# Kernel optimization log

Measured on AMD Instinct MI355X. Metric: run time of the kernel, lower is better.

Reference implementation:

```python
import jax, jax.numpy as jnp
import numpy as np

T, H, I, E, K = 4096, 2048, 1408, 8, 2  # tokens, hidden, intermediate, experts, top_k


def setup_inputs() -> dict:
    key = jax.random.key(0)
    ks = jax.random.split(key, 6)
    hidden_states = jax.random.normal(ks[0], (T, H), dtype=jnp.float32)
    gate_weight = jax.random.normal(ks[1], (E, H), dtype=jnp.float32) * 0.02  # fp32 gate, per source assert
    w13_weight = jax.random.randint(ks[2], (E, 2 * I, H), -127, 128, dtype=jnp.int8)
    w13_weight_scale = jax.random.uniform(ks[3], (E, 2 * I), dtype=jnp.float32, minval=0.5, maxval=1.5) * 0.005
    w2_weight = jax.random.randint(ks[4], (E, H, I), -127, 128, dtype=jnp.int8)
    w2_weight_scale = jax.random.uniform(ks[5], (E, H), dtype=jnp.float32, minval=0.5, maxval=1.5) * 0.005
    return dict(hidden_states=hidden_states, gate_weight=gate_weight,
                w13_weight=w13_weight, w13_weight_scale=w13_weight_scale,
                w2_weight=w2_weight, w2_weight_scale=w2_weight_scale)


def _dynamic_quant_i8(x):
    # per-token dynamic symmetric int8: scale = max|x|/127 (smooth scales default to ones)
    s = jnp.maximum(jnp.max(jnp.abs(x), axis=-1, keepdims=True) / 127.0, 1e-8)
    q = jnp.clip(jnp.round(x / s), -127.0, 127.0)
    return q, s


def reference(hidden_states, gate_weight, w13_weight, w13_weight_scale, w2_weight, w2_weight_scale):
    # --- gating: fp32 linear + topk softmax (renormalize=True) ---
    logits = hidden_states @ gate_weight.T              # [T, E]
    probs = jax.nn.softmax(logits, axis=-1)
    topv, topi = jax.lax.top_k(probs, K)                # [T, K]
    gates = topv / jnp.sum(topv, axis=-1, keepdims=True)
    # dense routing weights [T, E]: gate value where expert selected, else 0
    route = jnp.zeros((T, E), hidden_states.dtype).at[jnp.arange(T)[:, None], topi].add(gates)

    # --- dynamic per-token int8 quant of routed input (same token value for each of its K copies) ---
    q_in, s_in = _dynamic_quant_i8(hidden_states)       # [T, H], [T, 1]

    # --- grouped w8a8 GEMM (fc1) -> SwiGLU -> requant -> grouped GEMM (fc2) -> weighted combine ---
    def step(acc, xs):
        w13, s13, w2, s2w, r = xs                       # per-expert weights / route column [T]
        h1 = (q_in @ w13.T.astype(jnp.float32)) * s_in * s13[None, :]   # dequant fc1: [T, 2I]
        g, u = h1[:, :I], h1[:, I:]
        act = jax.nn.silu(g) * u                        # SwiGLU
        q_a, s_a = _dynamic_quant_i8(act)
        h2 = (q_a @ w2.T.astype(jnp.float32)) * s_a * s2w[None, :]      # dequant fc2: [T, H]
        return acc + r[:, None] * h2, None

    acc0 = jnp.zeros_like(hidden_states)
    out, _ = jax.lax.scan(step, acc0,
                          (w13_weight, w13_weight_scale, w2_weight, w2_weight_scale, route.T))
    return out
```

## Files before the change

kernel.cpp:

```cpp
#include <hip/hip_runtime.h>

#define T_TOK 4096
#define H_DIM 2048
#define I_DIM 1408
#define E_NUM 8
#define NI2   (2 * I_DIM)

typedef int v4i __attribute__((ext_vector_type(4)));

#define GLD_LDS16(gptr, lptr)                                                        \
  __builtin_amdgcn_global_load_lds(                                                  \
      (const __attribute__((address_space(1))) void*)(gptr),                         \
      (__attribute__((address_space(3))) void*)(lptr), 16, 0, 0)

__global__ __launch_bounds__(256) void pack_all(const int* __restrict__ w13,
                                                const int* __restrict__ w2,
                                                signed char* __restrict__ qw13,
                                                signed char* __restrict__ qw2,
                                                int n16a, int n16tot) {
  int i = blockIdx.x * 256 + threadIdx.x;
  if (i >= n16tot) return;
  const int* src;
  signed char* dst;
  int j;
  if (i < n16a) { src = w13; dst = qw13; j = i; }
  else          { src = w2;  dst = qw2;  j = i - n16a; }
  const int4* s4 = (const int4*)src + (size_t)j * 4;
  int4 v0 = s4[0], v1 = s4[1], v2 = s4[2], v3 = s4[3];
  union { signed char c[16]; int4 v; } pk;
  pk.c[0] = (signed char)v0.x;  pk.c[1] = (signed char)v0.y;
  pk.c[2] = (signed char)v0.z;  pk.c[3] = (signed char)v0.w;
  pk.c[4] = (signed char)v1.x;  pk.c[5] = (signed char)v1.y;
  pk.c[6] = (signed char)v1.z;  pk.c[7] = (signed char)v1.w;
  pk.c[8] = (signed char)v2.x;  pk.c[9] = (signed char)v2.y;
  pk.c[10] = (signed char)v2.z; pk.c[11] = (signed char)v2.w;
  pk.c[12] = (signed char)v3.x; pk.c[13] = (signed char)v3.y;
  pk.c[14] = (signed char)v3.z; pk.c[15] = (signed char)v3.w;
  ((int4*)dst)[j] = pk.v;
}

__global__ __launch_bounds__(256) void gate_route_quant(
    const float* __restrict__ hs, const float* __restrict__ gw,
    signed char* __restrict__ qin, float* __restrict__ s_in,
    int* __restrict__ tope, float* __restrict__ gts) {
  const int t = blockIdx.x;
  const int tid = threadIdx.x;
  const int lane = tid & 63;
  const int wave = tid >> 6;
  const float* row = hs + (size_t)t * H_DIM;

  const float4* r4 = (const float4*)row + tid * 2;
  float4 xa = r4[0], xb = r4[1];
  float x[8] = {xa.x, xa.y, xa.z, xa.w, xb.x, xb.y, xb.z, xb.w};

  double pd[8];
  for (int e = 0; e < 8; e++) pd[e] = 0.0;
  float am = 0.f;
  for (int j = 0; j < 8; j++) {
    float v = x[j];
    am = fmaxf(am, fabsf(v));
    int col = tid * 8 + j;
    for (int e = 0; e < 8; e++)
      pd[e] += (double)v * (double)gw[e * H_DIM + col];
  }
  for (int e = 0; e < 8; e++)
    for (int s = 32; s; s >>= 1) pd[e] += __shfl_down(pd[e], s);
  for (int s = 32; s; s >>= 1) am = fmaxf(am, __shfl_down(am, s));

  __shared__ double sred[4][8];
  __shared__ float sam[4];
  __shared__ float sbc;
  if (lane == 0) {
    for (int e = 0; e < 8; e++) sred[wave][e] = pd[e];
    sam[wave] = am;
  }
  __syncthreads();
  if (tid == 0) {
    float l[8];
    for (int e = 0; e < 8; e++)
      l[e] = (float)(sred[0][e] + sred[1][e] + sred[2][e] + sred[3][e]);
    float amx = fmaxf(fmaxf(sam[0], sam[1]), fmaxf(sam[2], sam[3]));
    float s = fmaxf(amx / 127.0f, 1e-8f);
    s_in[t] = s;
    sbc = s;
    int i1 = 0;
    for (int e = 1; e < 8; e++) if (l[e] > l[i1]) i1 = e;
    int i2 = -1;
    for (int e = 0; e < 8; e++) {
      if (e == i1) continue;
      if (i2 < 0 || l[e] > l[i2]) i2 = e;
    }
    float d = expf(l[i2] - l[i1]);
    tope[2 * t] = i1;     gts[2 * t] = 1.0f / (1.0f + d);
    tope[2 * t + 1] = i2; gts[2 * t + 1] = d / (1.0f + d);
  }
  __syncthreads();
  float s = sbc;
  union { signed char c[8]; unsigned long long u; } pk;
  for (int j = 0; j < 8; j++) {
    float q = rintf(x[j] / s);
    q = fminf(127.f, fmaxf(-127.f, q));
    pk.c[j] = (signed char)q;
  }
  ((unsigned long long*)(qin + (size_t)t * H_DIM))[tid] = pk.u;
}

__global__ __launch_bounds__(256) void build_lists(
    const int* __restrict__ tope, int* __restrict__ tok_list,
    int* __restrict__ epos, int* __restrict__ cnt) {
  const int e = blockIdx.x;
  const int tid = threadIdx.x;
  const int lane = tid & 63;
  const int wave = tid >> 6;
  __shared__ int wsum[4];
  __shared__ int base_s;
  if (tid == 0) base_s = 0;
  __syncthreads();
  for (int t0 = 0; t0 < T_TOK; t0 += 256) {
    int t = t0 + tid;
    int i1 = tope[2 * t], i2 = tope[2 * t + 1];
    int slot = (i1 == e) ? 0 : ((i2 == e) ? 1 : -1);
    unsigned long long m = __ballot(slot >= 0);
    int wpre = __popcll(m & ((1ull << lane) - 1ull));
    if (lane == 0) wsum[wave] = __popcll(m);
    __syncthreads();
    int pre = wpre;
    for (int w = 0; w < wave; w++) pre += wsum[w];
    int total = wsum[0] + wsum[1] + wsum[2] + wsum[3];
    int b = base_s;
    if (slot >= 0) {
      int pos = b + pre;
      tok_list[e * T_TOK + pos] = t;
      epos[2 * t + slot] = (e << 16) | pos;
    }
    __syncthreads();
    if (tid == 0) base_s = b + total;
  }
  __syncthreads();
  if (tid == 0) cnt[e] = base_s;
}

__global__ void calc_off(const int* __restrict__ cnt, int* __restrict__ off) {
  if (threadIdx.x == 0) {
    int s = 0;
    for (int e = 0; e < E_NUM; e++) { off[e] = s; s += cnt[e]; }
  }
}

__global__ __launch_bounds__(256, 3) void gemm1_silu(
    const signed char* __restrict__ qw13, const signed char* __restrict__ qin,
    const float* __restrict__ s_in, const float* __restrict__ s13,
    const int* __restrict__ tok_list, const int* __restrict__ cnt,
    const int* __restrict__ off, float* __restrict__ act,
    unsigned int* __restrict__ amax) {
  const int e = blockIdx.z;
  const int ce = cnt[e];
  const int m0 = blockIdx.y * 64;
  if (m0 >= ce) return;
  const int n0 = blockIdx.x * 128;

  __shared__ __align__(16) signed char As[64 * 64];
  __shared__ __align__(16) signed char Bg[128 * 64];
  __shared__ __align__(16) signed char Bu[128 * 64];

  const int tid = threadIdx.x;
  const int lane = tid & 63;
  const int wave = tid >> 6;
  const int quad = lane >> 4;
  const int ln = lane & 15;

  const int* tl = tok_list + e * T_TOK;
  const int rowA = tid >> 2;
  const int kc = (tid & 3) * 16;

  const int tA = tl[min(m0 + rowA, ce - 1)];
  const signed char* gA = qin + (size_t)tA * H_DIM + kc;
  const signed char* w13e = qw13 + (size_t)e * NI2 * H_DIM;
  const signed char* gBg0 = w13e + (size_t)(n0 + rowA) * H_DIM + kc;
  const signed char* gBg1 = w13e + (size_t)(n0 + rowA + 64) * H_DIM + kc;
  const signed char* gBu0 = gBg0 + (size_t)I_DIM * H_DIM;
  const signed char* gBu1 = gBg1 + (size_t)I_DIM * H_DIM;
  const int ldsA = tid * 16;
  const int lds1 = 4096 + ldsA;

  v4i accg[4][2], accu[4][2];
  v4i zero = {0, 0, 0, 0};
#pragma unroll
  for (int i = 0; i < 4; i++)
#pragma unroll
    for (int j = 0; j < 2; j++) { accg[i][j] = zero; accu[i][j] = zero; }

  for (int k0 = 0; k0 < H_DIM; k0 += 64) {
    __syncthreads();
    GLD_LDS16(gA + k0, As + ldsA);
    GLD_LDS16(gBg0 + k0, Bg + ldsA);
    GLD_LDS16(gBg1 + k0, Bg + lds1);
    GLD_LDS16(gBu0 + k0, Bu + ldsA);
    GLD_LDS16(gBu1 + k0, Bu + lds1);
    __syncthreads();

    v4i af[4], bgf[2], buf_[2];
#pragma unroll
    for (int mt = 0; mt < 4; mt++)
      af[mt] = *(const v4i*)(As + (mt * 16 + ln) * 64 + quad * 16);
#pragma unroll
    for (int nt = 0; nt < 2; nt++) {
      bgf[nt] = *(const v4i*)(Bg + (wave * 32 + nt * 16 + ln) * 64 + quad * 16);
      buf_[nt] = *(const v4i*)(Bu + (wave * 32 + nt * 16 + ln) * 64 + quad * 16);
    }
#pragma unroll
    for (int mt = 0; mt < 4; mt++)
#pragma unroll
      for (int nt = 0; nt < 2; nt++) {
        accg[mt][nt] = __builtin_amdgcn_mfma_i32_16x16x64_i8(af[mt], bgf[nt], accg[mt][nt], 0, 0, 0);
        accu[mt][nt] = __builtin_amdgcn_mfma_i32_16x16x64_i8(af[mt], buf_[nt], accu[mt][nt], 0, 0, 0);
      }
  }

  const float* s13e = s13 + e * NI2;
  float sg[2], su[2];
  int ncol[2];
#pragma unroll
  for (int nt = 0; nt < 2; nt++) {
    int n = n0 + wave * 32 + nt * 16 + ln;
    ncol[nt] = n;
    sg[nt] = s13e[n];
    su[nt] = s13e[I_DIM + n];
  }
  const int offe = off[e];
#pragma unroll
  for (int mt = 0; mt < 4; mt++) {
#pragma unroll
    for (int r = 0; r < 4; r++) {
      int mrel = m0 + mt * 16 + quad * 4 + r;
      bool valid = mrel < ce;
      int tok = tl[valid ? mrel : 0];
      float si = s_in[tok];
      int crow = offe + mrel;
      float* arow = act + (size_t)crow * I_DIM;
      float am = 0.f;
#pragma unroll
      for (int nt = 0; nt < 2; nt++) {
        float g = (float)accg[mt][nt][r] * si * sg[nt];
        float u = (float)accu[mt][nt][r] * si * su[nt];
        float a = g / (1.0f + expf(-g)) * u;
        if (valid) arow[ncol[nt]] = a;
        am = fmaxf(am, fabsf(a));
      }
      for (int s = 1; s < 16; s <<= 1) am = fmaxf(am, __shfl_xor(am, s, 16));
      if (valid && ln == 0) atomicMax(amax + crow, __float_as_uint(am));
    }
  }
}

__global__ __launch_bounds__(256) void quant_act(const float* __restrict__ act,
                                                 const unsigned int* __restrict__ amax,
                                                 signed char* __restrict__ qa,
                                                 float* __restrict__ s_a) {
  const int r = blockIdx.x;
  float am = __uint_as_float(amax[r]);
  float s = fmaxf(am / 127.0f, 1e-8f);
  if (threadIdx.x == 0) s_a[r] = s;
  const float* arow = act + (size_t)r * I_DIM;
  signed char* qrow = qa + (size_t)r * I_DIM;
  for (int j = threadIdx.x; j < I_DIM; j += 256) {
    float q = rintf(arow[j] / s);
    q = fminf(127.f, fmaxf(-127.f, q));
    qrow[j] = (signed char)q;
  }
}

__global__ __launch_bounds__(256, 4) void gemm2_h2(
    const signed char* __restrict__ qw2, const signed char* __restrict__ qa,
    const float* __restrict__ s_a, const float* __restrict__ s2w,
    const int* __restrict__ cnt, const int* __restrict__ off,
    float* __restrict__ h2s) {
  const int e = blockIdx.z;
  const int ce = cnt[e];
  const int m0 = blockIdx.y * 64;
  if (m0 >= ce) return;
  const int n0 = blockIdx.x * 128;
  const int offe = off[e];

  __shared__ __align__(16) signed char As[64 * 64];
  __shared__ __align__(16) signed char Bs[128 * 64];

  const int tid = threadIdx.x;
  const int lane = tid & 63;
  const int wave = tid >> 6;
  const int quad = lane >> 4;
  const int ln = lane & 15;

  const int rowA = tid >> 2;
  const int kc = (tid & 3) * 16;

  const signed char* gA = qa + (size_t)(offe + min(m0 + rowA, ce - 1)) * I_DIM + kc;
  const signed char* w2e = qw2 + (size_t)e * H_DIM * I_DIM;
  const signed char* gB0 = w2e + (size_t)(n0 + rowA) * I_DIM + kc;
  const signed char* gB1 = w2e + (size_t)(n0 + rowA + 64) * I_DIM + kc;
  const int ldsA = tid * 16;
  const int lds1 = 4096 + ldsA;

  v4i acc[4][2];
  v4i zero = {0, 0, 0, 0};
#pragma unroll
  for (int i = 0; i < 4; i++)
#pragma unroll
    for (int j = 0; j < 2; j++) acc[i][j] = zero;

  for (int k0 = 0; k0 < I_DIM; k0 += 64) {
    __syncthreads();
    GLD_LDS16(gA + k0, As + ldsA);
    GLD_LDS16(gB0 + k0, Bs + ldsA);
    GLD_LDS16(gB1 + k0, Bs + lds1);
    __syncthreads();

    v4i af[4], bf[2];
#pragma unroll
    for (int mt = 0; mt < 4; mt++)
      af[mt] = *(const v4i*)(As + (mt * 16 + ln) * 64 + quad * 16);
#pragma unroll
    for (int nt = 0; nt < 2; nt++)
      bf[nt] = *(const v4i*)(Bs + (wave * 32 + nt * 16 + ln) * 64 + quad * 16);
#pragma unroll
    for (int mt = 0; mt < 4; mt++)
#pragma unroll
      for (int nt = 0; nt < 2; nt++)
        acc[mt][nt] = __builtin_amdgcn_mfma_i32_16x16x64_i8(af[mt], bf[nt], acc[mt][nt], 0, 0, 0);
  }

  const float* s2e = s2w + e * H_DIM;
  float sw[2];
  int ncol[2];
#pragma unroll
  for (int nt = 0; nt < 2; nt++) {
    int n = n0 + wave * 32 + nt * 16 + ln;
    ncol[nt] = n;
    sw[nt] = s2e[n];
  }
#pragma unroll
  for (int mt = 0; mt < 4; mt++) {
#pragma unroll
    for (int r = 0; r < 4; r++) {
      int mrel = m0 + mt * 16 + quad * 4 + r;
      if (mrel >= ce) continue;
      float sa = s_a[offe + mrel];
      float* orow = h2s + (size_t)(offe + mrel) * H_DIM;
#pragma unroll
      for (int nt = 0; nt < 2; nt++)
        orow[ncol[nt]] = (float)acc[mt][nt][r] * sa * sw[nt];
    }
  }
}

__global__ __launch_bounds__(256) void gather_out(
    const float* __restrict__ h2s, const int* __restrict__ epos,
    const float* __restrict__ gts, const int* __restrict__ off,
    float* __restrict__ out) {
  const int t = blockIdx.x;
  int a = epos[2 * t], b = epos[2 * t + 1];
  float g1 = gts[2 * t], g2 = gts[2 * t + 1];
  int r1 = off[a >> 16] + (a & 0xffff);
  int r2 = off[b >> 16] + (b & 0xffff);
  const float4* R1 = (const float4*)(h2s + (size_t)r1 * H_DIM);
  const float4* R2 = (const float4*)(h2s + (size_t)r2 * H_DIM);
  float4* O = (float4*)(out + (size_t)t * H_DIM);
  for (int c = threadIdx.x; c < H_DIM / 4; c += 256) {
    float4 x = R1[c], y = R2[c];
    float4 z;
    z.x = g1 * x.x + g2 * y.x;
    z.y = g1 * x.y + g2 * y.y;
    z.z = g1 * x.z + g2 * y.z;
    z.w = g1 * x.w + g2 * y.w;
    O[c] = z;
  }
}

extern "C" void kernel_launch(void* const* d_in, const int* in_sizes, int n_in,
                              void* d_out, int out_size, void* d_ws, size_t ws_size,
                              hipStream_t stream) {
  const float* hs = (const float*)d_in[0];
  const float* gw = (const float*)d_in[1];
  const int* w13 = (const int*)d_in[2];
  const float* s13 = (const float*)d_in[3];
  const int* w2 = (const int*)d_in[4];
  const float* s2w = (const float*)d_in[5];
  float* out = (float*)d_out;

  char* ws = (char*)d_ws;
  size_t o = 0;
  auto take = [&](size_t b) {
    char* p = ws + o;
    o += (b + 255) & ~(size_t)255;
    return p;
  };
  signed char* qw13 = (signed char*)take((size_t)E_NUM * NI2 * H_DIM);
  signed char* qin = (signed char*)take((size_t)T_TOK * H_DIM);
  float* act = (float*)take((size_t)T_TOK * 2 * I_DIM * 4);
  float* h2s = (float*)qw13;
  signed char* qw2 = (signed char*)take((size_t)E_NUM * H_DIM * I_DIM);
  signed char* qa = (signed char*)take((size_t)T_TOK * 2 * I_DIM);
  float* sin_ = (float*)take((size_t)T_TOK * 4);
  float* sa = (float*)take((size_t)T_TOK * 2 * 4);
  unsigned int* amax = (unsigned int*)take((size_t)T_TOK * 2 * 4);
  int* tokl = (int*)take((size_t)E_NUM * T_TOK * 4);
  int* tope = (int*)take((size_t)T_TOK * 2 * 4);
  int* epos = (int*)take((size_t)T_TOK * 2 * 4);
  float* gts = (float*)take((size_t)T_TOK * 2 * 4);
  int* cnt = (int*)take(E_NUM * 4);
  int* off = (int*)take(E_NUM * 4);

  hipMemsetAsync(amax, 0, (size_t)T_TOK * 2 * 4, stream);

  {
    int n16a = E_NUM * NI2 * H_DIM / 16;
    int n16b = E_NUM * H_DIM * I_DIM / 16;
    int n16tot = n16a + n16b;
    pack_all<<<(n16tot + 255) / 256, 256, 0, stream>>>(w13, w2, qw13, qw2, n16a, n16tot);
  }
  gate_route_quant<<<T_TOK, 256, 0, stream>>>(hs, gw, qin, sin_, tope, gts);
  build_lists<<<E_NUM, 256, 0, stream>>>(tope, tokl, epos, cnt);
  calc_off<<<1, 64, 0, stream>>>(cnt, off);
  {
    dim3 g(I_DIM / 128, T_TOK / 64, E_NUM);
    gemm1_silu<<<g, 256, 0, stream>>>(qw13, qin, sin_, s13, tokl, cnt, off, act, amax);
  }
  quant_act<<<T_TOK * 2, 256, 0, stream>>>(act, amax, qa, sa);
  {
    dim3 g(H_DIM / 128, T_TOK / 64, E_NUM);
    gemm2_h2<<<g, 256, 0, stream>>>(qw2, qa, sa, s2w, cnt, off, h2s);
  }
  gather_out<<<T_TOK, 256, 0, stream>>>(h2s, epos, gts, off, out);
}
```

Baseline: 582.4 us.

## Parallelize list building and interleave experts in flattened GEMM grids

build_lists now runs one block per 256 tokens, using shared-memory atomics for per-expert slot positions and global atomics on a zeroed count array, replacing the sequential per-expert scan across all tokens. Both grouped GEMMs switch to a 1D grid with the expert index in the low bits, so blocks from different experts interleave and early-exiting empty tiles are spread out. gemm1 also halves its N tile to 64 columns and raises the occupancy hint to 4 blocks per CU, which gives more blocks for load balance but less B reuse per A load. Token order within each expert list becomes nondeterministic, which is harmless for correctness since positions are recorded in epos.

```diff
diff --git a/kernel.cpp b/kernel.cpp
--- a/kernel.cpp
+++ b/kernel.cpp
@@ -108,36 +108,24 @@
 __global__ __launch_bounds__(256) void build_lists(
     const int* __restrict__ tope, int* __restrict__ tok_list,
     int* __restrict__ epos, int* __restrict__ cnt) {
-  const int e = blockIdx.x;
+  __shared__ int lc[E_NUM];
+  __shared__ int lbase[E_NUM];
   const int tid = threadIdx.x;
-  const int lane = tid & 63;
-  const int wave = tid >> 6;
-  __shared__ int wsum[4];
-  __shared__ int base_s;
-  if (tid == 0) base_s = 0;
+  if (tid < E_NUM) lc[tid] = 0;
   __syncthreads();
-  for (int t0 = 0; t0 < T_TOK; t0 += 256) {
-    int t = t0 + tid;
-    int i1 = tope[2 * t], i2 = tope[2 * t + 1];
-    int slot = (i1 == e) ? 0 : ((i2 == e) ? 1 : -1);
-    unsigned long long m = __ballot(slot >= 0);
-    int wpre = __popcll(m & ((1ull << lane) - 1ull));
-    if (lane == 0) wsum[wave] = __popcll(m);
-    __syncthreads();
-    int pre = wpre;
-    for (int w = 0; w < wave; w++) pre += wsum[w];
-    int total = wsum[0] + wsum[1] + wsum[2] + wsum[3];
-    int b = base_s;
-    if (slot >= 0) {
-      int pos = b + pre;
-      tok_list[e * T_TOK + pos] = t;
-      epos[2 * t + slot] = (e << 16) | pos;
-    }
-    __syncthreads();
-    if (tid == 0) base_s = b + total;
-  }
+  const int t = blockIdx.x * 256 + tid;
+  int e0 = tope[2 * t], e1 = tope[2 * t + 1];
+  int p0 = atomicAdd(&lc[e0], 1);
+  int p1 = atomicAdd(&lc[e1], 1);
   __syncthreads();
-  if (tid == 0) cnt[e] = base_s;
+  if (tid < E_NUM) lbase[tid] = atomicAdd(&cnt[tid], lc[tid]);
+  __syncthreads();
+  int pos0 = lbase[e0] + p0;
+  int pos1 = lbase[e1] + p1;
+  tok_list[e0 * T_TOK + pos0] = t;
+  tok_list[e1 * T_TOK + pos1] = t;
+  epos[2 * t] = (e0 << 16) | pos0;
+  epos[2 * t + 1] = (e1 << 16) | pos1;
 }
 
 __global__ void calc_off(const int* __restrict__ cnt, int* __restrict__ off) {
@@ -147,21 +135,24 @@
   }
 }
 
-__global__ __launch_bounds__(256, 3) void gemm1_silu(
+__global__ __launch_bounds__(256, 4) void gemm1_silu(
     const signed char* __restrict__ qw13, const signed char* __restrict__ qin,
     const float* __restrict__ s_in, const float* __restrict__ s13,
     const int* __restrict__ tok_list, const int* __restrict__ cnt,
     const int* __restrict__ off, float* __restrict__ act,
     unsigned int* __restrict__ amax) {
-  const int e = blockIdx.z;
+  const int bid = blockIdx.x;
+  const int e = bid & 7;
+  const int xt = bid >> 9;
+  const int yt = (bid >> 3) & 63;
   const int ce = cnt[e];
-  const int m0 = blockIdx.y * 64;
+  const int m0 = yt * 64;
   if (m0 >= ce) return;
-  const int n0 = blockIdx.x * 128;
+  const int n0 = xt * 64;
 
   __shared__ __align__(16) signed char As[64 * 64];
-  __shared__ __align__(16) signed char Bg[128 * 64];
-  __shared__ __align__(16) signed char Bu[128 * 64];
+  __shared__ __align__(16) signed char Bg[64 * 64];
+  __shared__ __align__(16) signed char Bu[64 * 64];
 
   const int tid = threadIdx.x;
   const int lane = tid & 63;
@@ -176,57 +167,39 @@
   const int tA = tl[min(m0 + rowA, ce - 1)];
   const signed char* gA = qin + (size_t)tA * H_DIM + kc;
   const signed char* w13e = qw13 + (size_t)e * NI2 * H_DIM;
-  const signed char* gBg0 = w13e + (size_t)(n0 + rowA) * H_DIM + kc;
-  const signed char* gBg1 = w13e + (size_t)(n0 + rowA + 64) * H_DIM + kc;
-  const signed char* gBu0 = gBg0 + (size_t)I_DIM * H_DIM;
-  const signed char* gBu1 = gBg1 + (size_t)I_DIM * H_DIM;
+  const signed char* gBg = w13e + (size_t)(n0 + rowA) * H_DIM + kc;
+  const signed char* gBu = gBg + (size_t)I_DIM * H_DIM;
   const int ldsA = tid * 16;
-  const int lds1 = 4096 + ldsA;
-
-  v4i accg[4][2], accu[4][2];
+
+  v4i accg[4], accu[4];
   v4i zero = {0, 0, 0, 0};
 #pragma unroll
-  for (int i = 0; i < 4; i++)
-#pragma unroll
-    for (int j = 0; j < 2; j++) { accg[i][j] = zero; accu[i][j] = zero; }
+  for (int i = 0; i < 4; i++) { accg[i] = zero; accu[i] = zero; }
 
   for (int k0 = 0; k0 < H_DIM; k0 += 64) {
     __syncthreads();
     GLD_LDS16(gA + k0, As + ldsA);
-    GLD_LDS16(gBg0 + k0, Bg + ldsA);
-    GLD_LDS16(gBg1 + k0, Bg + lds1);
-    GLD_LDS16(gBu0 + k0, Bu + ldsA);
-    GLD_LDS16(gBu1 + k0, Bu + lds1);
+    GLD_LDS16(gBg + k0, Bg + ldsA);
+    GLD_LDS16(gBu + k0, Bu + ldsA);
     __syncthreads();
 
-    v4i af[4], bgf[2], buf_[2];
+    v4i af[4], bg, bu;
 #pragma unroll
     for (int mt = 0; mt < 4; mt++)
       af[mt] = *(const v4i*)(As + (mt * 16 + ln) * 64 + quad * 16);
-#pragma unroll
-    for (int nt = 0; nt < 2; nt++) {
-      bgf[nt] = *(const v4i*)(Bg + (wave * 32 + nt * 16 + ln) * 64 + quad * 16);
-      buf_[nt] = *(const v4i*)(Bu + (wave * 32 + nt * 16 + ln) * 64 + quad * 16);
+    bg = *(const v4i*)(Bg + (wave * 16 + ln) * 64 + quad * 16);
+    bu = *(const v4i*)(Bu + (wave * 16 + ln) * 64 + quad * 16);
+#pragma unroll
+    for (int mt = 0; mt < 4; mt++) {
+      accg[mt] = __builtin_amdgcn_mfma_i32_16x16x64_i8(af[mt], bg, accg[mt], 0, 0, 0);
+      accu[mt] = __builtin_amdgcn_mfma_i32_16x16x64_i8(af[mt], bu, accu[mt], 0, 0, 0);
     }
-#pragma unroll
-    for (int mt = 0; mt < 4; mt++)
-#pragma unroll
-      for (int nt = 0; nt < 2; nt++) {
-        accg[mt][nt] = __builtin_amdgcn_mfma_i32_16x16x64_i8(af[mt], bgf[nt], accg[mt][nt], 0, 0, 0);
-        accu[mt][nt] = __builtin_amdgcn_mfma_i32_16x16x64_i8(af[mt], buf_[nt], accu[mt][nt], 0, 0, 0);
-      }
   }
 
   const float* s13e = s13 + e * NI2;
-  float sg[2], su[2];
-  int ncol[2];
-#pragma unroll
-  for (int nt = 0; nt < 2; nt++) {
-    int n = n0 + wave * 32 + nt * 16 + ln;
-    ncol[nt] = n;
-    sg[nt] = s13e[n];
-    su[nt] = s13e[I_DIM + n];
-  }
+  const int n = n0 + wave * 16 + ln;
+  const float sgv = s13e[n];
+  const float suv = s13e[I_DIM + n];
   const int offe = off[e];
 #pragma unroll
   for (int mt = 0; mt < 4; mt++) {
@@ -237,16 +210,11 @@
       int tok = tl[valid ? mrel : 0];
       float si = s_in[tok];
       int crow = offe + mrel;
-      float* arow = act + (size_t)crow * I_DIM;
-      float am = 0.f;
-#pragma unroll
-      for (int nt = 0; nt < 2; nt++) {
-        float g = (float)accg[mt][nt][r] * si * sg[nt];
-        float u = (float)accu[mt][nt][r] * si * su[nt];
-        float a = g / (1.0f + expf(-g)) * u;
-        if (valid) arow[ncol[nt]] = a;
-        am = fmaxf(am, fabsf(a));
-      }
+      float g = (float)accg[mt][r] * si * sgv;
+      float u = (float)accu[mt][r] * si * suv;
+      float a = g / (1.0f + expf(-g)) * u;
+      if (valid) act[(size_t)crow * I_DIM + n] = a;
+      float am = fabsf(a);
       for (int s = 1; s < 16; s <<= 1) am = fmaxf(am, __shfl_xor(am, s, 16));
       if (valid && ln == 0) atomicMax(amax + crow, __float_as_uint(am));
     }
@@ -275,11 +243,14 @@
     const float* __restrict__ s_a, const float* __restrict__ s2w,
     const int* __restrict__ cnt, const int* __restrict__ off,
     float* __restrict__ h2s) {
-  const int e = blockIdx.z;
+  const int bid = blockIdx.x;
+  const int e = bid & 7;
+  const int xt = bid >> 9;
+  const int yt = (bid >> 3) & 63;
   const int ce = cnt[e];
-  const int m0 = blockIdx.y * 64;
+  const int m0 = yt * 64;
   if (m0 >= ce) return;
-  const int n0 = blockIdx.x * 128;
+  const int n0 = xt * 128;
   const int offe = off[e];
 
   __shared__ __align__(16) signed char As[64 * 64];
@@ -297,7 +268,7 @@
   const signed char* gA = qa + (size_t)(offe + min(m0 + rowA, ce - 1)) * I_DIM + kc;
   const signed char* w2e = qw2 + (size_t)e * H_DIM * I_DIM;
   const signed char* gB0 = w2e + (size_t)(n0 + rowA) * I_DIM + kc;
-  const signed char* gB1 = w2e + (size_t)(n0 + rowA + 64) * I_DIM + kc;
+  const signed char* gB1 = gB0 + (size_t)64 * I_DIM;
   const int ldsA = tid * 16;
   const int lds1 = 4096 + ldsA;
 
@@ -411,6 +382,7 @@
   int* off = (int*)take(E_NUM * 4);
 
   hipMemsetAsync(amax, 0, (size_t)T_TOK * 2 * 4, stream);
+  hipMemsetAsync(cnt, 0, (size_t)E_NUM * 4, stream);
 
   {
     int n16a = E_NUM * NI2 * H_DIM / 16;
@@ -419,16 +391,10 @@
     pack_all<<<(n16tot + 255) / 256, 256, 0, stream>>>(w13, w2, qw13, qw2, n16a, n16tot);
   }
   gate_route_quant<<<T_TOK, 256, 0, stream>>>(hs, gw, qin, sin_, tope, gts);
-  build_lists<<<E_NUM, 256, 0, stream>>>(tope, tokl, epos, cnt);
+  build_lists<<<T_TOK / 256, 256, 0, stream>>>(tope, tokl, epos, cnt);
   calc_off<<<1, 64, 0, stream>>>(cnt, off);
-  {
-    dim3 g(I_DIM / 128, T_TOK / 64, E_NUM);
-    gemm1_silu<<<g, 256, 0, stream>>>(qw13, qin, sin_, s13, tokl, cnt, off, act, amax);
-  }
+  gemm1_silu<<<(I_DIM / 64) * 64 * E_NUM, 256, 0, stream>>>(qw13, qin, sin_, s13, tokl, cnt, off, act, amax);
   quant_act<<<T_TOK * 2, 256, 0, stream>>>(act, amax, qa, sa);
-  {
-    dim3 g(H_DIM / 128, T_TOK / 64, E_NUM);
-    gemm2_h2<<<g, 256, 0, stream>>>(qw2, qa, sa, s2w, cnt, off, h2s);
-  }
+  gemm2_h2<<<(H_DIM / 128) * 64 * E_NUM, 256, 0, stream>>>(qw2, qa, sa, s2w, cnt, off, h2s);
   gather_out<<<T_TOK, 256, 0, stream>>>(h2s, epos, gts, off, out);
 }
```

Measured after the change: 586.1 us. About the same (+0.6%).
